# Performance work log

Measured on AMD Instinct MI355X. Metric: run time of the kernel, lower is better.

Reference implementation:

```python
import jax, jax.numpy as jnp
import numpy as np

N_EMBD = 1024
N_HEAD = 16
HEAD_DIM = N_EMBD // N_HEAD


def setup_inputs() -> dict:
    key = jax.random.key(0)
    k1, k2, k3, k4, k5 = jax.random.split(key, 5)
    x = jax.random.normal(k1, (4, 2048, N_EMBD), dtype=jnp.float32)
    s = 1.0 / np.sqrt(N_EMBD)
    W_attn = jax.random.normal(k2, (N_EMBD, 3 * N_EMBD), dtype=jnp.float32) * s
    b_attn = jnp.zeros((3 * N_EMBD,), dtype=jnp.float32)
    W_proj = jax.random.normal(k3, (N_EMBD, N_EMBD), dtype=jnp.float32) * s
    b_proj = jnp.zeros((N_EMBD,), dtype=jnp.float32)
    return {"x": x, "W_attn": W_attn, "b_attn": b_attn, "W_proj": W_proj, "b_proj": b_proj}


def _attention(x, W_attn, b_attn, W_proj, b_proj):
    B, T, C = x.shape
    qkv = jnp.einsum("btc,cd->btd", x, W_attn) + b_attn  # [B,T,3C]
    q, k, v = jnp.split(qkv, 3, axis=-1)
    # [B,T,C] -> [B,H,T,D]
    def heads(t):
        return t.reshape(B, T, N_HEAD, HEAD_DIM).transpose(0, 2, 1, 3)
    q, k, v = heads(q), heads(k), heads(v)
    scale = 1.0 / np.sqrt(HEAD_DIM)
    scores = jnp.einsum("bhqd,bhkd->bhqk", q, k) * scale  # [B,H,T,T]
    causal = jnp.tril(jnp.ones((T, T), dtype=bool))
    scores = jnp.where(causal, scores, jnp.finfo(scores.dtype).min)
    attn = jax.nn.softmax(scores, axis=-1)
    y = jnp.einsum("bhqk,bhkd->bhqd", attn, v)  # [B,H,T,D]
    y = y.transpose(0, 2, 1, 3).reshape(B, T, C)
    return jnp.einsum("btc,cd->btd", y, W_proj) + b_proj


def reference(x, W_attn, b_attn, W_proj, b_proj):
    return _attention(x, W_attn, b_attn, W_proj, b_proj)
```

## Files before the change

### kernel.cpp

```cpp
#include <hip/hip_runtime.h>
#include <hip/hip_bf16.h>

#define BB 4
#define TT 2048
#define CC 1024
#define HH 16
#define DD 64
#define BT (BB*TT)
#define C3 (3*CC)
#define LDST 72
#define QSCALE 0.18033688011112042f

typedef __attribute__((ext_vector_type(8))) short short8;
typedef __attribute__((ext_vector_type(4))) float f32x4;

__device__ __forceinline__ short f2bs(float f) {
  __hip_bfloat16 h = __float2bfloat16(f);
  return *reinterpret_cast<short*>(&h);
}

__device__ __forceinline__ void gl_lds16(const short* g, short* l) {
  __builtin_amdgcn_global_load_lds(
      (const __attribute__((address_space(1))) void*)(g),
      (__attribute__((address_space(3))) void*)(l), 16, 0, 0);
}

__global__ __launch_bounds__(256)
void prep(const float* __restrict__ Wa, short* __restrict__ Wat,
          const float* __restrict__ Wp, short* __restrict__ Wpt,
          const float* __restrict__ x, short* __restrict__ Xb)
{
  __shared__ float Lt[64][65];
  const int bx = blockIdx.x;
  if (bx >= 64) {
    size_t chunk = (size_t)(bx - 64) * 16 + blockIdx.y;
    size_t i = (chunk * 256 + threadIdx.x) * 8;
    float4 a = *reinterpret_cast<const float4*>(x + i);
    float4 b = *reinterpret_cast<const float4*>(x + i + 4);
    short8 o;
    o[0] = f2bs(a.x); o[1] = f2bs(a.y); o[2] = f2bs(a.z); o[3] = f2bs(a.w);
    o[4] = f2bs(b.x); o[5] = f2bs(b.y); o[6] = f2bs(b.z); o[7] = f2bs(b.w);
    *reinterpret_cast<short8*>(Xb + i) = o;
    return;
  }
  const bool isA = (bx < 48);
  const float* in  = isA ? Wa  : Wp;
  short*       out = isA ? Wat : Wpt;
  const int N  = isA ? C3 : CC;
  const int n0 = (isA ? bx : bx - 48) * 64;
  const int k0 = blockIdx.y * 64;
  const int cx = threadIdx.x & 15, rr = threadIdx.x >> 4;
#pragma unroll
  for (int p = 0; p < 4; ++p) {
    int kr = p * 16 + rr;
    float4 u = *reinterpret_cast<const float4*>(in + (size_t)(k0 + kr) * N + n0 + cx * 4);
    Lt[kr][cx * 4 + 0] = u.x;
    Lt[kr][cx * 4 + 1] = u.y;
    Lt[kr][cx * 4 + 2] = u.z;
    Lt[kr][cx * 4 + 3] = u.w;
  }
  __syncthreads();
#pragma unroll
  for (int p = 0; p < 4; ++p) {
    int nr = p * 16 + rr;
    short4 o;
    o.x = f2bs(Lt[cx * 4 + 0][nr]);
    o.y = f2bs(Lt[cx * 4 + 1][nr]);
    o.z = f2bs(Lt[cx * 4 + 2][nr]);
    o.w = f2bs(Lt[cx * 4 + 3][nr]);
    *reinterpret_cast<short4*>(out + (size_t)(n0 + nr) * CC + k0 + cx * 4) = o;
  }
}

template<bool QKV>
__global__ __launch_bounds__(256, 2)
void gemm128(const short* __restrict__ A, const short* __restrict__ Bt,
             const float* __restrict__ bias,
             short* __restrict__ qb, short* __restrict__ kb, short* __restrict__ vb,
             float* __restrict__ out)
{
  __shared__ __align__(16) short SMEM[32768];

  const int t = threadIdx.x;
  const int lane = t & 63;
  const int l16 = lane & 15, quad = lane >> 4;
  const int w = t >> 6;
  const int wm = w & 1, wn = w >> 1;

  const int per   = gridDim.x >> 3;
  const int chunk = (blockIdx.x & 7) * per + (blockIdx.x >> 3);
  const int NBC   = QKV ? 24 : 8;
  const int row0  = (chunk / NBC) * 128;
  const int col0  = (chunk % NBC) * 128;

  auto stageQA = [&](int bufS, int kcS, int tileS) __attribute__((always_inline)) {
#pragma unroll
    for (int l = 0; l < 2; ++l) {
      int gq = l * 256 + t;
      int rq = gq >> 2;
      int g  = (gq & 3) ^ ((rq >> 1) & 3);
      gl_lds16(A + (size_t)(row0 + rq) * CC + tileS * 64 + kcS * 32 + g * 8,
               &SMEM[bufS * 8192 + kcS * 4096 + gq * 8]);
    }
  };
  auto stageQB = [&](int bufS, int kcS, int tileS) __attribute__((always_inline)) {
#pragma unroll
    for (int l = 0; l < 2; ++l) {
      int gq = l * 256 + t;
      int rq = gq >> 2;
      int g  = (gq & 3) ^ ((rq >> 1) & 3);
      gl_lds16(Bt + (size_t)(col0 + rq) * CC + tileS * 64 + kcS * 32 + g * 8,
               &SMEM[16384 + bufS * 8192 + kcS * 4096 + gq * 8]);
    }
  };

  f32x4 acc[4][4];
#pragma unroll
  for (int i = 0; i < 4; ++i)
#pragma unroll
    for (int j = 0; j < 4; ++j) acc[i][j] = (f32x4){0.f, 0.f, 0.f, 0.f};

  auto kTile = [&](int u, int cb, int tm) __attribute__((always_inline)) {
    const short* Ac = &SMEM[cb * 8192];
    const short* Bc = &SMEM[16384 + cb * 8192];
    short8 bf[4];
#pragma unroll
    for (int ph = 0; ph < 4; ++ph) {
      const int kc = ph >> 1, q = ph & 1;
      if (q == 0) {
#pragma unroll
        for (int j = 0; j < 4; ++j) {
          int rb = wn * 64 + j * 16 + l16;
          bf[j] = *reinterpret_cast<const short8*>(
              &Bc[kc * 4096 + rb * 32 + (((quad ^ (rb >> 1)) & 3) << 3)]);
        }
      }
      short8 af[2];
#pragma unroll
      for (int iq = 0; iq < 2; ++iq) {
        int ra = wm * 64 + (q * 2 + iq) * 16 + l16;
        af[iq] = *reinterpret_cast<const short8*>(
            &Ac[kc * 4096 + ra * 32 + (((quad ^ (ra >> 1)) & 3) << 3)]);
      }

      if      (ph == 0) { if (tm < 2) stageQA(cb ^ 1, 1, u + 1); }
      else if (ph == 1) { if (tm < 2) stageQB(cb ^ 1, 1, u + 1); }
      else if (ph == 2) { if (tm < 1) stageQA(cb,     0, u + 2); }
      else              { if (tm < 1) stageQB(cb,     0, u + 2); }

      __builtin_amdgcn_s_barrier();
      asm volatile("s_waitcnt lgkmcnt(0)" ::: "memory");
      __builtin_amdgcn_sched_barrier(0);

      __builtin_amdgcn_s_setprio(1);
#pragma unroll
      for (int iq = 0; iq < 2; ++iq)
#pragma unroll
        for (int j = 0; j < 4; ++j)
          acc[q * 2 + iq][j] =
              __builtin_amdgcn_mfma_f32_16x16x32_bf16(af[iq], bf[j], acc[q * 2 + iq][j], 0, 0, 0);
      __builtin_amdgcn_s_setprio(0);

      if (ph == 1) {
        if (tm == 2) { asm volatile("s_waitcnt vmcnt(0)" ::: "memory"); }
        else         { asm volatile("s_waitcnt vmcnt(8)" ::: "memory"); }
      } else if (ph == 3) {
        if      (tm == 0) { asm volatile("s_waitcnt vmcnt(8)" ::: "memory"); }
        else if (tm == 1) { asm volatile("s_waitcnt vmcnt(4)" ::: "memory"); }
      }
      __builtin_amdgcn_s_barrier();
    }
  };

  stageQA(0, 0, 0);  stageQB(0, 0, 0);
  stageQA(0, 1, 0);  stageQB(0, 1, 0);
  stageQA(1, 0, 1);  stageQB(1, 0, 1);
  asm volatile("s_waitcnt vmcnt(8)" ::: "memory");
  __builtin_amdgcn_s_barrier();

  for (int u = 0; u < 14; u += 2) {
    kTile(u,     0, 0);
    kTile(u + 1, 1, 0);
  }
  kTile(14, 0, 1);
  kTile(15, 1, 2);

  if constexpr (QKV) {
    const int sel = col0 >> 10;
    const int bi  = row0 >> 11;
#pragma unroll
    for (int j = 0; j < 4; ++j) {
      const int colL = wn * 64 + j * 16 + l16;
      const float bv = bias[col0 + colL];
#pragma unroll
      for (int i = 0; i < 4; ++i)
#pragma unroll
        for (int r = 0; r < 4; ++r) {
          const int rl = wm * 64 + i * 16 + quad * 4 + r;
          float val = acc[i][j][r] + bv;
          if (sel == 0) val *= QSCALE;
          short vs = f2bs(val);
          if (sel == 2) {
            int tpl = (rl & ~63) | ((rl & 15) << 2) | ((rl >> 4) & 3);
            SMEM[colL * 136 + tpl] = vs;
          } else {
            SMEM[rl * 136 + colL] = vs;
          }
        }
    }
    __syncthreads();
    if (sel == 0) {
#pragma unroll
      for (int rep = 0; rep < 8; ++rep) {
        int slot = rep * 256 + t;
        int rl = slot >> 4, ch = slot & 15;
        short8 vv = *reinterpret_cast<const short8*>(&SMEM[rl * 136 + ch * 8]);
        int tt  = (row0 & 2047) + rl;
        int cin = (col0 + ch * 8) & 1023;
        int hh = cin >> 6, dd = cin & 63;
        *reinterpret_cast<short8*>(
            &qb[(((size_t)(bi * HH + hh)) * TT + tt) * DD + dd]) = vv;
      }
    } else if (sel == 1) {
#pragma unroll
      for (int rep = 0; rep < 8; ++rep) {
        int slot = rep * 256 + t;
        int rl = slot >> 4, ch = slot & 15;
        short8 vv = *reinterpret_cast<const short8*>(&SMEM[rl * 136 + ch * 8]);
        int tt  = (row0 & 2047) + rl;
        int cin = (col0 + ch * 8) & 1023;
        int hh = cin >> 6;
        int rt = tt & 63;
        int cs = ((cin >> 3) & 7) ^ ((rt >> 1) & 7);
        size_t tile = (size_t)(bi * HH + hh) * 32 + (tt >> 6);
        *reinterpret_cast<short8*>(&kb[tile * 4096 + rt * 64 + cs * 8]) = vv;
      }
    } else {
#pragma unroll
      for (int rep = 0; rep < 8; ++rep) {
        int slot = rep * 256 + t;
        int dcol = slot >> 4, ch = slot & 15;
        short8 vv = *reinterpret_cast<const short8*>(&SMEM[dcol * 136 + ch * 8]);
        int cin = (col0 + dcol) & 1023;
        int hh = cin >> 6, dd = cin & 63;
        int ktv = ((row0 & 2047) >> 6) + (ch >> 3);
        int cs  = (ch & 7) ^ ((dd >> 1) & 7);
        *reinterpret_cast<short8*>(
            &vb[((size_t)(bi * HH + hh) * 32 + ktv) * 4096 + dd * 64 + cs * 8]) = vv;
      }
    }
  } else {
#pragma unroll
    for (int j = 0; j < 4; ++j) {
      int col = col0 + wn * 64 + j * 16 + l16;
      float bv = bias[col];
#pragma unroll
      for (int i = 0; i < 4; ++i)
#pragma unroll
        for (int r = 0; r < 4; ++r) {
          int row = row0 + wm * 64 + i * 16 + quad * 4 + r;
          out[(size_t)row * CC + col] = acc[i][j][r] + bv;
        }
    }
  }
}

__global__ __launch_bounds__(256, 2)
void attn_mfma(const short* __restrict__ Qb, const short* __restrict__ Kb,
               const short* __restrict__ Vb, short* __restrict__ Y)
{
  __shared__ __align__(16) short Kd[2][4096];
  __shared__ __align__(16) short Vt[4096];
  __shared__ __align__(16) short Pw[4 * 32 * LDST];

  const int t    = threadIdx.x;
  const int w    = t >> 6;
  const int lane = t & 63;
  const int l16  = lane & 15;
  const int quad = lane >> 4;

  const int linear = blockIdx.x + 8 * (blockIdx.y + 16 * blockIdx.z);
  const int nb  = (linear & 7) * 64 + (linear >> 3);
  const int qb0 = nb & 7;
  const int h   = (nb >> 3) & 15;
  const int bi  = nb >> 7;
  const size_t head = (size_t)(bi * HH + h) * TT * DD;

  short* myP = &Pw[w * 32 * LDST];

  auto stageK = [&](int kt, int p) __attribute__((always_inline)) {
    const short* src = Kb + head + (size_t)kt * 4096;
    gl_lds16(src + t * 8,        &Kd[p][t * 8]);
    gl_lds16(src + 2048 + t * 8, &Kd[p][2048 + t * 8]);
  };
  auto stageV = [&](int kt) __attribute__((always_inline)) {
    const short* src = Vb + head + (size_t)kt * 4096;
    gl_lds16(src + t * 8,        &Vt[t * 8]);
    gl_lds16(src + 2048 + t * 8, &Vt[2048 + t * 8]);
  };

  const int qbs[2] = { qb0, 15 - qb0 };

#pragma unroll
  for (int half = 0; half < 2; ++half) {
    const int qb  = qbs[half];
    const int q0  = qb * 128;
    const int nkt = 2 * qb + 2;

    short8 qf[2][2];
#pragma unroll
    for (int i = 0; i < 2; ++i)
#pragma unroll
      for (int kc = 0; kc < 2; ++kc)
        qf[i][kc] = *reinterpret_cast<const short8*>(
            &Qb[head + (size_t)(q0 + w * 32 + i * 16 + l16) * DD + kc * 32 + quad * 8]);

    f32x4 O[2][4];
#pragma unroll
    for (int i = 0; i < 2; ++i)
#pragma unroll
      for (int dt = 0; dt < 4; ++dt) O[i][dt] = (f32x4){0.f, 0.f, 0.f, 0.f};
    float lsum[2][4] = {};

    stageK(0, 0);
    stageV(0);
    stageK(1, 1);
    asm volatile("s_waitcnt vmcnt(4)" ::: "memory");
    __builtin_amdgcn_s_barrier();

    for (int kt = 0; kt < nkt; ++kt) {
      const int p  = kt & 1;
      const int k0 = kt * 64;

      short8 kf[4][2];
#pragma unroll
      for (int nt = 0; nt < 4; ++nt)
#pragma unroll
        for (int kc = 0; kc < 2; ++kc) {
          int r = nt * 16 + l16;
          int c = kc * 4 + quad;
          kf[nt][kc] = *reinterpret_cast<const short8*>(
              &Kd[p][r * 64 + ((c ^ ((r >> 1) & 7)) << 3)]);
        }

      f32x4 s[2][4];
#pragma unroll
      for (int i = 0; i < 2; ++i)
#pragma unroll
        for (int nt = 0; nt < 4; ++nt) s[i][nt] = (f32x4){0.f, 0.f, 0.f, 0.f};
      __builtin_amdgcn_s_setprio(1);
#pragma unroll
      for (int i = 0; i < 2; ++i)
#pragma unroll
        for (int nt = 0; nt < 4; ++nt)
#pragma unroll
          for (int kc = 0; kc < 2; ++kc)
            s[i][nt] = __builtin_amdgcn_mfma_f32_16x16x32_bf16(qf[i][kc], kf[nt][kc], s[i][nt], 0, 0, 0);
      __builtin_amdgcn_s_setprio(0);

#pragma unroll
      for (int i = 0; i < 2; ++i) {
        const int rowg_base = q0 + w * 32 + i * 16 + quad * 4;
#pragma unroll
        for (int r = 0; r < 4; ++r) {
          const int rowg = rowg_base + r;
          short pk[4];
#pragma unroll
          for (int nt = 0; nt < 4; ++nt) {
            float e = (k0 + nt * 16 + l16 <= rowg) ? __builtin_amdgcn_exp2f(s[i][nt][r]) : 0.f;
            lsum[i][r] += e;
            pk[nt] = f2bs(e);
          }
          short4 p4; p4.x = pk[0]; p4.y = pk[1]; p4.z = pk[2]; p4.w = pk[3];
          *reinterpret_cast<short4*>(&myP[(i * 16 + quad * 4 + r) * LDST + (l16 << 2)]) = p4;
        }
      }

      asm volatile("s_waitcnt vmcnt(0)" ::: "memory");
      __builtin_amdgcn_s_barrier();

      if (kt + 2 < nkt) stageK(kt + 2, p);

      __builtin_amdgcn_s_setprio(1);
#pragma unroll
      for (int cc = 0; cc < 2; ++cc) {
        short8 pf[2];
#pragma unroll
        for (int i = 0; i < 2; ++i)
          pf[i] = *reinterpret_cast<const short8*>(
              &myP[(i * 16 + l16) * LDST + cc * 32 + quad * 8]);
#pragma unroll
        for (int dt = 0; dt < 4; ++dt) {
          int r = dt * 16 + l16;
          int c = cc * 4 + quad;
          short8 vf = *reinterpret_cast<const short8*>(
              &Vt[r * 64 + ((c ^ ((r >> 1) & 7)) << 3)]);
#pragma unroll
          for (int i = 0; i < 2; ++i)
            O[i][dt] = __builtin_amdgcn_mfma_f32_16x16x32_bf16(pf[i], vf, O[i][dt], 0, 0, 0);
        }
      }
      __builtin_amdgcn_s_setprio(0);

      __builtin_amdgcn_s_barrier();
      if (kt + 1 < nkt) stageV(kt + 1);
    }

    float linv[2][4];
#pragma unroll
    for (int i = 0; i < 2; ++i)
#pragma unroll
      for (int r = 0; r < 4; ++r) {
        float s = lsum[i][r];
        s += __shfl_xor(s, 1);
        s += __shfl_xor(s, 2);
        s += __shfl_xor(s, 4);
        s += __shfl_xor(s, 8);
        linv[i][r] = 1.f / s;
      }
#pragma unroll
    for (int i = 0; i < 2; ++i)
#pragma unroll
      for (int dt = 0; dt < 4; ++dt)
#pragma unroll
        for (int r = 0; r < 4; ++r) {
          int tg = q0 + w * 32 + i * 16 + quad * 4 + r;
          Y[((size_t)bi * TT + tg) * CC + h * DD + dt * 16 + l16] =
              f2bs(O[i][dt][r] * linv[i][r]);
        }
  }
}

extern "C" void kernel_launch(void* const* d_in, const int* in_sizes, int n_in,
                              void* d_out, int out_size, void* d_ws, size_t ws_size,
                              hipStream_t stream) {
  const float* x  = (const float*)d_in[0];
  const float* Wa = (const float*)d_in[1];
  const float* ba = (const float*)d_in[2];
  const float* Wp = (const float*)d_in[3];
  const float* bp = (const float*)d_in[4];
  float* out = (float*)d_out;

  const size_t NELT = (size_t)BB * HH * TT * DD;
  short* qb  = (short*)d_ws;
  short* kb  = qb + NELT;
  short* vb  = kb + NELT;
  short* Xb  = vb + NELT;
  short* Wat = Xb  + (size_t)BT * CC;
  short* Wpt = Wat + (size_t)CC * C3;
  short* Yb  = Wpt + (size_t)CC * CC;

  prep<<<dim3(64 + 256, 16), 256, 0, stream>>>(Wa, Wat, Wp, Wpt, x, Xb);

  gemm128<true> <<<dim3((BT / 128) * (C3 / 128)), 256, 0, stream>>>(Xb, Wat, ba, qb, kb, vb, nullptr);
  attn_mfma     <<<dim3(8, HH, BB),               256, 0, stream>>>(qb, kb, vb, Yb);
  gemm128<false><<<dim3((BT / 128) * (CC / 128)), 256, 0, stream>>>(Yb, Wpt, bp, nullptr, nullptr, nullptr, out);
}
```

Before: 241.7 us.

## Restructure GEMM k-tile into two phases and remap blocks to XCD row groups

The GEMM k-tile loop now loads all four A fragments and four B fragments per 32-wide k-chunk and issues 16 MFMAs per phase. That halves the phases per tile and drops one workgroup barrier per phase. The block-to-tile mapping also changes so that each XCD owns a contiguous group of 8 row tiles and walks across the column tiles, aiming for better L2 reuse of A rows. The cost is more live fragment registers and larger global-load bursts per phase. There is also less interleaving of LDS reads with MFMA work.

```diff
diff --git a/kernel.cpp b/kernel.cpp
--- a/kernel.cpp
+++ b/kernel.cpp
@@ -87,11 +87,10 @@
   const int w = t >> 6;
   const int wm = w & 1, wn = w >> 1;
 
-  const int per   = gridDim.x >> 3;
-  const int chunk = (blockIdx.x & 7) * per + (blockIdx.x >> 3);
-  const int NBC   = QKV ? 24 : 8;
-  const int row0  = (chunk / NBC) * 128;
-  const int col0  = (chunk % NBC) * 128;
+  const int xcd   = blockIdx.x & 7;
+  const int idx   = blockIdx.x >> 3;
+  const int row0  = (xcd * 8 + (idx & 7)) * 128;
+  const int col0  = (idx >> 3) * 128;
 
   auto stageQA = [&](int bufS, int kcS, int tileS) __attribute__((always_inline)) {
 #pragma unroll
@@ -123,48 +122,43 @@
   auto kTile = [&](int u, int cb, int tm) __attribute__((always_inline)) {
     const short* Ac = &SMEM[cb * 8192];
     const short* Bc = &SMEM[16384 + cb * 8192];
-    short8 bf[4];
-#pragma unroll
-    for (int ph = 0; ph < 4; ++ph) {
-      const int kc = ph >> 1, q = ph & 1;
-      if (q == 0) {
-#pragma unroll
-        for (int j = 0; j < 4; ++j) {
-          int rb = wn * 64 + j * 16 + l16;
-          bf[j] = *reinterpret_cast<const short8*>(
-              &Bc[kc * 4096 + rb * 32 + (((quad ^ (rb >> 1)) & 3) << 3)]);
-        }
-      }
-      short8 af[2];
-#pragma unroll
-      for (int iq = 0; iq < 2; ++iq) {
-        int ra = wm * 64 + (q * 2 + iq) * 16 + l16;
-        af[iq] = *reinterpret_cast<const short8*>(
+#pragma unroll
+    for (int kc = 0; kc < 2; ++kc) {
+      short8 af[4], bf[4];
+#pragma unroll
+      for (int j = 0; j < 4; ++j) {
+        int rb = wn * 64 + j * 16 + l16;
+        bf[j] = *reinterpret_cast<const short8*>(
+            &Bc[kc * 4096 + rb * 32 + (((quad ^ (rb >> 1)) & 3) << 3)]);
+      }
+#pragma unroll
+      for (int i = 0; i < 4; ++i) {
+        int ra = wm * 64 + i * 16 + l16;
+        af[i] = *reinterpret_cast<const short8*>(
             &Ac[kc * 4096 + ra * 32 + (((quad ^ (ra >> 1)) & 3) << 3)]);
       }
 
-      if      (ph == 0) { if (tm < 2) stageQA(cb ^ 1, 1, u + 1); }
-      else if (ph == 1) { if (tm < 2) stageQB(cb ^ 1, 1, u + 1); }
-      else if (ph == 2) { if (tm < 1) stageQA(cb,     0, u + 2); }
-      else              { if (tm < 1) stageQB(cb,     0, u + 2); }
-
-      __builtin_amdgcn_s_barrier();
+      if (kc == 0) {
+        if (tm < 2) { stageQA(cb ^ 1, 1, u + 1); stageQB(cb ^ 1, 1, u + 1); }
+      } else {
+        if (tm < 1) { stageQA(cb,     0, u + 2); stageQB(cb,     0, u + 2); }
+      }
+
       asm volatile("s_waitcnt lgkmcnt(0)" ::: "memory");
       __builtin_amdgcn_sched_barrier(0);
 
       __builtin_amdgcn_s_setprio(1);
 #pragma unroll
-      for (int iq = 0; iq < 2; ++iq)
+      for (int i = 0; i < 4; ++i)
 #pragma unroll
         for (int j = 0; j < 4; ++j)
-          acc[q * 2 + iq][j] =
-              __builtin_amdgcn_mfma_f32_16x16x32_bf16(af[iq], bf[j], acc[q * 2 + iq][j], 0, 0, 0);
+          acc[i][j] = __builtin_amdgcn_mfma_f32_16x16x32_bf16(af[i], bf[j], acc[i][j], 0, 0, 0);
       __builtin_amdgcn_s_setprio(0);
 
-      if (ph == 1) {
+      if (kc == 0) {
         if (tm == 2) { asm volatile("s_waitcnt vmcnt(0)" ::: "memory"); }
         else         { asm volatile("s_waitcnt vmcnt(8)" ::: "memory"); }
-      } else if (ph == 3) {
+      } else {
         if      (tm == 0) { asm volatile("s_waitcnt vmcnt(8)" ::: "memory"); }
         else if (tm == 1) { asm volatile("s_waitcnt vmcnt(4)" ::: "memory"); }
       }
```

New measurement: 232.9 us. 3.6% less time.
